# Kernel optimization log

Hardware: AMD Instinct MI355X
Metric: run time of the kernel (lower is better)

Reference implementation:

```python
import jax, jax.numpy as jnp
import numpy as np

N, E, D_IN, H, C = 50000, 800000, 128, 4, 32  # C = out_channels // heads

def setup_inputs() -> dict:
    key = jax.random.key(0)
    k1, k2, k3, k4, k5, k6, k7 = jax.random.split(key, 7)
    x = jax.random.normal(k1, (N, D_IN), dtype=jnp.float32)
    # edges guaranteed self-loop-free (matches remove_self_loops on the torch side)
    src = jax.random.randint(k2, (E,), 0, N)
    off = jax.random.randint(k3, (E,), 1, N)
    dst = (src + off) % N
    edge_index = jnp.stack([src, dst]).astype(jnp.int64)
    W = jax.random.normal(k4, (D_IN, H * C), dtype=jnp.float32) * 0.05
    b_lin = jax.random.normal(k5, (H * C,), dtype=jnp.float32) * 0.05
    att = jax.random.normal(k6, (1, H, 2 * C), dtype=jnp.float32) * 0.1
    bias = jnp.zeros((H * C,), dtype=jnp.float32)
    return {"x": x, "edge_index": edge_index, "W": W, "b_lin": b_lin, "att": att, "bias": bias}

def reference(x, edge_index, W, b_lin, att, bias):
    n = x.shape[0]
    # add self loops (every segment nonempty -> safe segment_max)
    loops = jnp.tile(jnp.arange(n, dtype=edge_index.dtype)[None, :], (2, 1))
    ei = jnp.concatenate([edge_index, loops], axis=1)
    e_i, e_j = ei[0], ei[1]  # e_i: destination (softmax/scatter group), e_j: source
    h = (x @ W + b_lin).reshape(n, H, C)  # [N,H,C]
    x_i = h[e_i]  # [E',H,C]
    x_j = h[e_j]
    # attention logits: split att into its x_i / x_j halves to avoid a concat
    a_i, a_j = att[..., :C], att[..., C:]
    logits = (x_i * a_i).sum(-1) + (x_j * a_j).sum(-1)  # [E',H]
    logits = jax.nn.leaky_relu(logits, negative_slope=0.2)
    # segment softmax over destination nodes
    seg_max = jax.ops.segment_max(logits, e_i, num_segments=n)  # [N,H]
    ex = jnp.exp(logits - seg_max[e_i])
    seg_sum = jax.ops.segment_sum(ex, e_i, num_segments=n)
    alpha = ex / seg_sum[e_i]  # [E',H]
    # weighted scatter-sum aggregation
    out = jax.ops.segment_sum(alpha[:, :, None] * x_j, e_i, num_segments=n)  # [N,H,C]
    out = out.reshape(n, H * C) + bias  # concat=True
    return jax.nn.relu(out)
```

## Files before the change

kernel.cpp:

```cpp
#include <hip/hip_runtime.h>
#include <hip/hip_bf16.h>

#define DIN 128
#define HC  128
#define NH  4

typedef __attribute__((ext_vector_type(8))) short short8;
typedef __attribute__((ext_vector_type(4))) float floatx4;

__device__ inline short f2bf_bits(float f) {
    __hip_bfloat16 t = __float2bfloat16(f);
    return *reinterpret_cast<short*>(&t);
}
__device__ inline float bfbits2f(unsigned short u) {
    union { unsigned int i; float f; } c; c.i = ((unsigned int)u) << 16; return c.f;
}

__global__ __launch_bounds__(256) void zero_deg(int* __restrict__ deg, int n)
{
    const int i = blockIdx.x * 256 + threadIdx.x;
    if (i < n) deg[i] = 0;
}

#define GB 256
#define CB 1024
__global__ __launch_bounds__(256) void gemm_count(
    const float* __restrict__ x, const float* __restrict__ W,
    const float* __restrict__ b, const float* __restrict__ att,
    __hip_bfloat16* __restrict__ h, float* __restrict__ ali,
    float* __restrict__ alj,
    const int* __restrict__ src, int* __restrict__ deg,
    unsigned short* __restrict__ rank,
    int n, int ntiles, int E, int total)
{
    __shared__ __hip_bfloat16 Wt[DIN][136];

    if (blockIdx.x >= GB) {
        for (int e = (blockIdx.x - GB) * 256 + threadIdx.x; e < total;
             e += CB * 256) {
            const int i = (e < E) ? src[e] : (e - E);
            rank[e] = (unsigned short)atomicAdd(&deg[i], 1);
        }
        return;
    }

    for (int idx = threadIdx.x; idx < DIN * HC; idx += 256) {
        const int k = idx >> 7, c = idx & 127;
        Wt[c][k] = __float2bfloat16(W[idx]);
    }
    __syncthreads();

    const int lane = threadIdx.x & 63;
    const int l15 = lane & 15, lg = lane >> 4;

    short8 bf[8][4];
    #pragma unroll
    for (int ct = 0; ct < 8; ++ct)
        #pragma unroll
        for (int ks = 0; ks < 4; ++ks)
            bf[ct][ks] = *(const short8*)(&Wt[ct * 16 + l15][ks * 32 + lg * 8]);

    float bc[8], ai_l[8], aj_l[8];
    #pragma unroll
    for (int ct = 0; ct < 8; ++ct) {
        bc[ct]   = b[ct * 16 + l15];
        ai_l[ct] = att[(ct >> 1) * 64 + (ct & 1) * 16 + l15];
        aj_l[ct] = att[(ct >> 1) * 64 + 32 + (ct & 1) * 16 + l15];
    }

    const int gw = (blockIdx.x * 256 + threadIdx.x) >> 6;
    const int nw = (GB * 256) >> 6;
    for (int tile = gw; tile < ntiles; tile += nw) {
        int row = tile * 16 + l15;
        if (row >= n) row = n - 1;
        floatx4 acc[8];
        #pragma unroll
        for (int ct = 0; ct < 8; ++ct) acc[ct] = (floatx4)0.f;

        #pragma unroll
        for (int ks = 0; ks < 4; ++ks) {
            const float4 f0 = *(const float4*)(x + (size_t)row * DIN + ks * 32 + lg * 8);
            const float4 f1 = *(const float4*)(x + (size_t)row * DIN + ks * 32 + lg * 8 + 4);
            short8 af;
            af[0] = f2bf_bits(f0.x); af[1] = f2bf_bits(f0.y);
            af[2] = f2bf_bits(f0.z); af[3] = f2bf_bits(f0.w);
            af[4] = f2bf_bits(f1.x); af[5] = f2bf_bits(f1.y);
            af[6] = f2bf_bits(f1.z); af[7] = f2bf_bits(f1.w);
            #pragma unroll
            for (int ct = 0; ct < 8; ++ct)
                acc[ct] = __builtin_amdgcn_mfma_f32_16x16x32_bf16(
                    af, bf[ct][ks], acc[ct], 0, 0, 0);
        }

        #pragma unroll
        for (int reg = 0; reg < 4; ++reg) {
            const int r = tile * 16 + lg * 4 + reg;

            #pragma unroll
            for (int ct = 0; ct < 8; ++ct)
                if (r < n)
                    h[(size_t)r * HC + ct * 16 + l15] =
                        __float2bfloat16(acc[ct][reg] + bc[ct]);

            float pi[4], pj[4];
            #pragma unroll
            for (int hd = 0; hd < 4; ++hd) {
                float vi = 0.f, vj = 0.f;
                #pragma unroll
                for (int q = 0; q < 2; ++q) {
                    const int ct = hd * 2 + q;
                    const float hv = acc[ct][reg] + bc[ct];
                    vi = fmaf(hv, ai_l[ct], vi);
                    vj = fmaf(hv, aj_l[ct], vj);
                }
                #pragma unroll
                for (int m = 1; m <= 8; m <<= 1) {
                    vi += __shfl_xor(vi, m);
                    vj += __shfl_xor(vj, m);
                }
                pi[hd] = vi; pj[hd] = vj;
            }
            if (l15 < 8 && r < n) {
                const int hd = l15 & 3;
                float wi = pi[0];
                wi = (hd == 1) ? pi[1] : wi;
                wi = (hd == 2) ? pi[2] : wi;
                wi = (hd == 3) ? pi[3] : wi;
                float wj = pj[0];
                wj = (hd == 1) ? pj[1] : wj;
                wj = (hd == 2) ? pj[2] : wj;
                wj = (hd == 3) ? pj[3] : wj;
                if (l15 < 4) ali[(size_t)r * 4 + hd] = wi;
                else         alj[(size_t)r * 4 + hd] = wj;
            }
        }
    }
}

__global__ __launch_bounds__(256) void scan1(
    const int* __restrict__ deg, int* __restrict__ rowptr,
    int* __restrict__ bsum, int n)
{
    __shared__ int sh[256];
    const int t = threadIdx.x;
    const int i = blockIdx.x * 256 + t;
    const int v = (i < n) ? deg[i] : 0;
    sh[t] = v;
    __syncthreads();
    #pragma unroll
    for (int off = 1; off < 256; off <<= 1) {
        const int u = (t >= off) ? sh[t - off] : 0;
        __syncthreads();
        sh[t] += u;
        __syncthreads();
    }
    if (i < n) rowptr[i] = sh[t] - v;
    if (t == 255) bsum[blockIdx.x] = sh[255];
}

__global__ __launch_bounds__(1024) void scan2(
    const int* __restrict__ bsum, int* __restrict__ boff, int nb)
{
    __shared__ int sh[1024];
    const int t = threadIdx.x;
    const int v = (t < nb) ? bsum[t] : 0;
    sh[t] = v;
    __syncthreads();
    #pragma unroll
    for (int off = 1; off < 1024; off <<= 1) {
        const int u = (t >= off) ? sh[t - off] : 0;
        __syncthreads();
        sh[t] += u;
        __syncthreads();
    }
    if (t < nb) boff[t] = sh[t] - v;
}

__global__ __launch_bounds__(256) void scatter_edges(
    const int* __restrict__ src, const int* __restrict__ dst,
    const unsigned short* __restrict__ rank, const int* __restrict__ rowptr,
    const int* __restrict__ boff, unsigned short* __restrict__ csr,
    int E, int total)
{
    const int e = blockIdx.x * 256 + threadIdx.x;
    if (e >= total) return;
    int i, j;
    if (e < E) { i = src[e]; j = dst[e]; }
    else       { i = e - E;  j = i; }
    csr[rowptr[i] + boff[i >> 8] + (int)rank[e]] = (unsigned short)j;
}

__global__ __launch_bounds__(256) void aggregate_csr(
    const int* __restrict__ rowptr, const int* __restrict__ boff,
    const unsigned short* __restrict__ csr,
    const float* __restrict__ ali, const float* __restrict__ alj,
    const __hip_bfloat16* __restrict__ h, const float* __restrict__ bias,
    float* __restrict__ out, int n, int total)
{
    const int lane = threadIdx.x & 63;
    const int hh   = lane >> 4;
    const int gw = (blockIdx.x * 256 + threadIdx.x) >> 6;
    const int nw = (gridDim.x * 256) >> 6;
    const unsigned short* hu = (const unsigned short*)h;
    const float b0 = bias[lane * 2], b1 = bias[lane * 2 + 1];

    for (int i = gw; i < n; i += nw) {
        const int rs = rowptr[i] + boff[i >> 8];
        const int re = (i + 1 == n) ? total
                                    : rowptr[i + 1] + boff[(i + 1) >> 8];
        const float aii = ali[(size_t)i * 4 + hh];

        float acc0 = 0.f, acc1 = 0.f, s = 0.f;
        int t = rs;
        for (; t + 8 <= re; t += 8) {
            int jj[8]; float ll[8]; ushort2 uu[8];
            #pragma unroll
            for (int q = 0; q < 8; ++q) jj[q] = csr[t + q];
            #pragma unroll
            for (int q = 0; q < 8; ++q) ll[q] = alj[(size_t)jj[q] * 4 + hh];
            #pragma unroll
            for (int q = 0; q < 8; ++q)
                uu[q] = *(const ushort2*)(hu + (size_t)jj[q] * HC + lane * 2);
            #pragma unroll
            for (int q = 0; q < 8; ++q) {
                float l = aii + ll[q];
                l = l > 0.f ? l : 0.2f * l;
                const float ex = __expf(l);
                s += ex;
                acc0 = fmaf(ex, bfbits2f(uu[q].x), acc0);
                acc1 = fmaf(ex, bfbits2f(uu[q].y), acc1);
            }
        }
        for (; t + 4 <= re; t += 4) {
            int jj[4]; float ll[4]; ushort2 uu[4];
            #pragma unroll
            for (int q = 0; q < 4; ++q) jj[q] = csr[t + q];
            #pragma unroll
            for (int q = 0; q < 4; ++q) ll[q] = alj[(size_t)jj[q] * 4 + hh];
            #pragma unroll
            for (int q = 0; q < 4; ++q)
                uu[q] = *(const ushort2*)(hu + (size_t)jj[q] * HC + lane * 2);
            #pragma unroll
            for (int q = 0; q < 4; ++q) {
                float l = aii + ll[q];
                l = l > 0.f ? l : 0.2f * l;
                const float ex = __expf(l);
                s += ex;
                acc0 = fmaf(ex, bfbits2f(uu[q].x), acc0);
                acc1 = fmaf(ex, bfbits2f(uu[q].y), acc1);
            }
        }
        for (; t < re; ++t) {
            const int j = csr[t];
            float l = aii + alj[(size_t)j * 4 + hh];
            l = l > 0.f ? l : 0.2f * l;
            const float ex = __expf(l);
            s += ex;
            const ushort2 u = *(const ushort2*)(hu + (size_t)j * HC + lane * 2);
            acc0 = fmaf(ex, bfbits2f(u.x), acc0);
            acc1 = fmaf(ex, bfbits2f(u.y), acc1);
        }
        const float inv = 1.0f / s;
        float o0 = fmaf(acc0, inv, b0);
        float o1 = fmaf(acc1, inv, b1);
        float2 ov;
        ov.x = o0 > 0.f ? o0 : 0.f;
        ov.y = o1 > 0.f ? o1 : 0.f;
        *(float2*)(out + (size_t)i * HC + lane * 2) = ov;
    }
}

extern "C" void kernel_launch(void* const* d_in, const int* in_sizes, int n_in,
                              void* d_out, int out_size, void* d_ws, size_t ws_size,
                              hipStream_t stream)
{
    const float* x    = (const float*)d_in[0];
    const int*   ei   = (const int*)d_in[1];
    const float* W    = (const float*)d_in[2];
    const float* b    = (const float*)d_in[3];
    const float* att  = (const float*)d_in[4];
    const float* bias = (const float*)d_in[5];

    const int n     = in_sizes[0] / DIN;
    const int E     = in_sizes[1] / 2;
    const int total = E + n;

    const int* src = ei;
    const int* dst = ei + E;

    char* ws = (char*)d_ws;
    size_t off = 0;
    auto take = [&](size_t bytes) {
        char* p = ws + off;
        off += (bytes + 255) & ~(size_t)255;
        return p;
    };
    const int nb = (n + 255) / 256;
    __hip_bfloat16* h   = (__hip_bfloat16*)take((size_t)n * HC * 2);
    float* ali    = (float*)take((size_t)n * NH * 4);
    float* alj    = (float*)take((size_t)n * NH * 4);
    int*   rowptr = (int*)take((size_t)(n + 1) * 4);
    int*   deg    = (int*)take((size_t)n * 4);
    int*   bsum   = (int*)take((size_t)nb * 4);
    int*   boff   = (int*)take((size_t)nb * 4);
    unsigned short* rank = (unsigned short*)take((size_t)total * 2);
    unsigned short* csr  = (unsigned short*)take((size_t)total * 2);

    float* out = (float*)d_out;

    zero_deg<<<nb, 256, 0, stream>>>(deg, n);

    const int ntiles = (n + 15) / 16;
    gemm_count<<<GB + CB, 256, 0, stream>>>(x, W, b, att, h, ali, alj,
                                            src, deg, rank, n, ntiles, E, total);

    scan1<<<nb, 256, 0, stream>>>(deg, rowptr, bsum, n);
    scan2<<<1, 1024, 0, stream>>>(bsum, boff, nb);

    const int eb = (total + 255) / 256;
    scatter_edges<<<eb, 256, 0, stream>>>(src, dst, rank, rowptr, boff, csr,
                                          E, total);

    const int nodeBlocks = (n + 3) / 4;
    aggregate_csr<<<nodeBlocks, 256, 0, stream>>>(rowptr, boff, csr, ali, alj,
                                                  h, bias, out, n, total);
}
```

Measured before the change: 106.4 us.

## Replace global atomic degree counting with per-chunk LDS histograms

Degree counting switches from global atomics on a deg array to LDS histograms, one block per (edge chunk, node range) pair. The per-chunk counts are written to a cnt matrix, and scan1 turns them into per-chunk offsets. The scatter then adds chunk offset plus local rank to find each edge's slot, and the zero_deg launch is dropped. This removes global atomic contention, but every histogram block rereads its whole 64K-edge chunk once per node range (8x src reads), and scan1 now loops serially over the chunks for each node.

```diff
diff --git a/kernel.cpp b/kernel.cpp
--- a/kernel.cpp
+++ b/kernel.cpp
@@ -5,6 +5,11 @@
 #define HC  128
 #define NH  4
 
+#define GB        256
+#define RANGES    8
+#define CHUNK_LOG 16
+#define CNK       (1 << CHUNK_LOG)
+
 typedef __attribute__((ext_vector_type(8))) short short8;
 typedef __attribute__((ext_vector_type(4))) float floatx4;
 
@@ -16,34 +21,40 @@
     union { unsigned int i; float f; } c; c.i = ((unsigned int)u) << 16; return c.f;
 }
 
-__global__ __launch_bounds__(256) void zero_deg(int* __restrict__ deg, int n)
-{
-    const int i = blockIdx.x * 256 + threadIdx.x;
-    if (i < n) deg[i] = 0;
-}
-
-#define GB 256
-#define CB 1024
 __global__ __launch_bounds__(256) void gemm_count(
     const float* __restrict__ x, const float* __restrict__ W,
     const float* __restrict__ b, const float* __restrict__ att,
     __hip_bfloat16* __restrict__ h, float* __restrict__ ali,
     float* __restrict__ alj,
-    const int* __restrict__ src, int* __restrict__ deg,
-    unsigned short* __restrict__ rank,
-    int n, int ntiles, int E, int total)
-{
-    __shared__ __hip_bfloat16 Wt[DIN][136];
+    const int* __restrict__ src, unsigned short* __restrict__ cnt,
+    unsigned short* __restrict__ rank16,
+    int n, int ntiles, int E, int total, int rsize)
+{
+    __shared__ __align__(16) unsigned char smem[DIN * 136 * 2];
 
     if (blockIdx.x >= GB) {
-        for (int e = (blockIdx.x - GB) * 256 + threadIdx.x; e < total;
-             e += CB * 256) {
+        int* hist = (int*)smem;
+        const int hb = blockIdx.x - GB;
+        const int c = hb >> 3, r = hb & (RANGES - 1);
+        const int base = r * rsize;
+        const int sz = min(base + rsize, n) - base;
+        for (int u = threadIdx.x; u < sz; u += 256) hist[u] = 0;
+        __syncthreads();
+        const int e0 = c << CHUNK_LOG;
+        const int e1 = min(e0 + CNK, total);
+        for (int e = e0 + threadIdx.x; e < e1; e += 256) {
             const int i = (e < E) ? src[e] : (e - E);
-            rank[e] = (unsigned short)atomicAdd(&deg[i], 1);
-        }
+            const unsigned u = (unsigned)(i - base);
+            if (u < (unsigned)sz)
+                rank16[e] = (unsigned short)atomicAdd(&hist[u], 1);
+        }
+        __syncthreads();
+        for (int u = threadIdx.x; u < sz; u += 256)
+            cnt[(size_t)c * n + base + u] = (unsigned short)hist[u];
         return;
     }
 
+    auto Wt = reinterpret_cast<__hip_bfloat16(*)[136]>(smem);
     for (int idx = threadIdx.x; idx < DIN * HC; idx += 256) {
         const int k = idx >> 7, c = idx & 127;
         Wt[c][k] = __float2bfloat16(W[idx]);
@@ -138,14 +149,22 @@
 }
 
 __global__ __launch_bounds__(256) void scan1(
-    const int* __restrict__ deg, int* __restrict__ rowptr,
-    int* __restrict__ bsum, int n)
+    unsigned short* __restrict__ cnt, int* __restrict__ rowptr,
+    int* __restrict__ bsum, int n, int nchunks)
 {
     __shared__ int sh[256];
     const int t = threadIdx.x;
     const int i = blockIdx.x * 256 + t;
-    const int v = (i < n) ? deg[i] : 0;
-    sh[t] = v;
+    int run = 0;
+    if (i < n) {
+        for (int c = 0; c < nchunks; ++c) {
+            const size_t idx = (size_t)c * n + i;
+            const int v = cnt[idx];
+            cnt[idx] = (unsigned short)run;
+            run += v;
+        }
+    }
+    sh[t] = run;
     __syncthreads();
     #pragma unroll
     for (int off = 1; off < 256; off <<= 1) {
@@ -154,7 +173,7 @@
         sh[t] += u;
         __syncthreads();
     }
-    if (i < n) rowptr[i] = sh[t] - v;
+    if (i < n) rowptr[i] = sh[t] - run;
     if (t == 255) bsum[blockIdx.x] = sh[255];
 }
 
@@ -178,16 +197,20 @@
 
 __global__ __launch_bounds__(256) void scatter_edges(
     const int* __restrict__ src, const int* __restrict__ dst,
-    const unsigned short* __restrict__ rank, const int* __restrict__ rowptr,
-    const int* __restrict__ boff, unsigned short* __restrict__ csr,
-    int E, int total)
+    const unsigned short* __restrict__ rank16,
+    const unsigned short* __restrict__ cnt,
+    const int* __restrict__ rowptr, const int* __restrict__ boff,
+    unsigned short* __restrict__ csr, int E, int total, int n)
 {
     const int e = blockIdx.x * 256 + threadIdx.x;
     if (e >= total) return;
     int i, j;
     if (e < E) { i = src[e]; j = dst[e]; }
     else       { i = e - E;  j = i; }
-    csr[rowptr[i] + boff[i >> 8] + (int)rank[e]] = (unsigned short)j;
+    const int pos = rowptr[i] + boff[i >> 8]
+                  + (int)cnt[(size_t)(e >> CHUNK_LOG) * n + i]
+                  + (int)rank16[e];
+    csr[pos] = (unsigned short)j;
 }
 
 __global__ __launch_bounds__(256) void aggregate_csr(
@@ -288,6 +311,10 @@
     const int* src = ei;
     const int* dst = ei + E;
 
+    const int nchunks = (total + CNK - 1) >> CHUNK_LOG;
+    const int rsize   = (n + RANGES - 1) / RANGES;
+    const int nb      = (n + 255) / 256;
+
     char* ws = (char*)d_ws;
     size_t off = 0;
     auto take = [&](size_t bytes) {
@@ -295,31 +322,29 @@
         off += (bytes + 255) & ~(size_t)255;
         return p;
     };
-    const int nb = (n + 255) / 256;
     __hip_bfloat16* h   = (__hip_bfloat16*)take((size_t)n * HC * 2);
     float* ali    = (float*)take((size_t)n * NH * 4);
     float* alj    = (float*)take((size_t)n * NH * 4);
     int*   rowptr = (int*)take((size_t)(n + 1) * 4);
-    int*   deg    = (int*)take((size_t)n * 4);
     int*   bsum   = (int*)take((size_t)nb * 4);
     int*   boff   = (int*)take((size_t)nb * 4);
-    unsigned short* rank = (unsigned short*)take((size_t)total * 2);
-    unsigned short* csr  = (unsigned short*)take((size_t)total * 2);
+    unsigned short* cnt    = (unsigned short*)take((size_t)nchunks * n * 2);
+    unsigned short* rank16 = (unsigned short*)take((size_t)total * 2);
+    unsigned short* csr    = (unsigned short*)take((size_t)total * 2);
 
     float* out = (float*)d_out;
 
-    zero_deg<<<nb, 256, 0, stream>>>(deg, n);
-
     const int ntiles = (n + 15) / 16;
-    gemm_count<<<GB + CB, 256, 0, stream>>>(x, W, b, att, h, ali, alj,
-                                            src, deg, rank, n, ntiles, E, total);
-
-    scan1<<<nb, 256, 0, stream>>>(deg, rowptr, bsum, n);
+    gemm_count<<<GB + nchunks * RANGES, 256, 0, stream>>>(
+        x, W, b, att, h, ali, alj, src, cnt, rank16,
+        n, ntiles, E, total, rsize);
+
+    scan1<<<nb, 256, 0, stream>>>(cnt, rowptr, bsum, n, nchunks);
     scan2<<<1, 1024, 0, stream>>>(bsum, boff, nb);
 
     const int eb = (total + 255) / 256;
-    scatter_edges<<<eb, 256, 0, stream>>>(src, dst, rank, rowptr, boff, csr,
-                                          E, total);
+    scatter_edges<<<eb, 256, 0, stream>>>(src, dst, rank16, cnt, rowptr, boff,
+                                          csr, E, total, n);
 
     const int nodeBlocks = (n + 3) / 4;
     aggregate_csr<<<nodeBlocks, 256, 0, stream>>>(rowptr, boff, csr, ali, alj,
```

New measurement: 157.5 us. 48.0% more time.
